# Kernel tuning notes

Measured on AMD Instinct MI355X. Metric: run time of the kernel, lower is better.

Reference implementation:

```python
import jax, jax.numpy as jnp
import numpy as np

N_SRC0, N_DST0 = 500000, 65536
N_DST1 = 8192
E0, E1 = 1048576, 131072
H = 4
SLOPE = 0.2


def gat_conv(h_src, h_dst, src, dst, Ws, Wd, al, ar, b, n_dst, act):
    # h_src: [Ns, Fin], Ws: [Fin, H*D]
    D = Ws.shape[1] // H
    fs = (h_src @ Ws).reshape(-1, H, D)          # [Ns,H,D]
    fd = (h_dst @ Wd).reshape(-1, H, D)          # [Nd,H,D]
    el = jnp.einsum('nhd,hd->nh', fs, al)        # [Ns,H]
    er = jnp.einsum('nhd,hd->nh', fd, ar)        # [Nd,H]
    e = jax.nn.leaky_relu(el[src] + er[dst], SLOPE)   # [E,H]
    m = jax.ops.segment_max(e, dst, num_segments=n_dst, indices_are_sorted=True)
    a = jnp.exp(e - m[dst])                      # [E,H]
    s = jax.ops.segment_sum(a, dst, num_segments=n_dst, indices_are_sorted=True)
    alpha = a / s[dst]                           # [E,H]
    msg = fs[src] * alpha[..., None]             # [E,H,D]
    out = jax.ops.segment_sum(msg, dst, num_segments=n_dst, indices_are_sorted=True) + b
    return act(out)                              # [Nd,H,D]


def setup_inputs() -> dict:
    key = jax.random.key(0)
    ks = jax.random.split(key, 16)
    D0, D1 = 64, 47
    inp = {
        'x': jax.random.normal(ks[0], (N_SRC0, 128), jnp.float32),
        'src0': jax.random.randint(ks[1], (E0,), 0, N_SRC0, jnp.int32),
        'dst0': jnp.sort(jax.random.randint(ks[2], (E0,), 0, N_DST0, jnp.int32)),
        'src1': jax.random.randint(ks[3], (E1,), 0, N_DST0, jnp.int32),
        'dst1': jnp.sort(jax.random.randint(ks[4], (E1,), 0, N_DST1, jnp.int32)),
        'Ws0': jax.random.normal(ks[5], (128, H * D0), jnp.float32) * 0.05,
        'Wd0': jax.random.normal(ks[6], (128, H * D0), jnp.float32) * 0.05,
        'al0': jax.random.normal(ks[7], (H, D0), jnp.float32) * 0.05,
        'ar0': jax.random.normal(ks[8], (H, D0), jnp.float32) * 0.05,
        'b0': jax.random.normal(ks[9], (H, D0), jnp.float32) * 0.05,
        'Ws1': jax.random.normal(ks[10], (H * D0, H * D1), jnp.float32) * 0.05,
        'Wd1': jax.random.normal(ks[11], (H * D0, H * D1), jnp.float32) * 0.05,
        'al1': jax.random.normal(ks[12], (H, D1), jnp.float32) * 0.05,
        'ar1': jax.random.normal(ks[13], (H, D1), jnp.float32) * 0.05,
        'b1': jax.random.normal(ks[14], (H, D1), jnp.float32) * 0.05,
    }
    return inp


def reference(x, src0, dst0, src1, dst1, Ws0, Wd0, al0, ar0, b0, Ws1, Wd1, al1, ar1, b1):
    # Layer 0: bipartite GATConv with ReLU, flatten heads
    h_dst = x[:N_DST0]
    h = gat_conv(x, h_dst, src0, dst0, Ws0, Wd0, al0, ar0, b0, N_DST0, jax.nn.relu)
    h = h.reshape(N_DST0, -1)                    # [N_DST0, H*D0]
    # Layer 1: no activation, mean over heads, log_softmax
    h_dst = h[:N_DST1]
    h = gat_conv(h, h_dst, src1, dst1, Ws1, Wd1, al1, ar1, b1, N_DST1, lambda z: z)
    h = h.mean(axis=1)                           # [N_DST1, D1]
    return jax.nn.log_softmax(h, axis=-1)
```

## Files before the change

### kernel.cpp

```cpp
#include <hip/hip_runtime.h>

typedef _Float16 half8  __attribute__((ext_vector_type(8)));
typedef _Float16 half4v __attribute__((ext_vector_type(4)));
typedef float    f32x4  __attribute__((ext_vector_type(4)));

#define GAT_SLOPE 0.2f
#define N_SRC0 500000
#define N_DST0 65536
#define N_DST1 8192
#define E0 1048576
#define E1 131072
#define H 4
#define MAXSEG 80

__device__ __forceinline__ float leaky(float x) { return x >= 0.f ? x : GAT_SLOPE * x; }

__global__ void collapse_kernel(const float* __restrict__ W, const float* __restrict__ a,
                                float* __restrict__ out, int K, int D) {
  int i = blockIdx.x * 256 + threadIdx.x;
  if (i >= K * 4) return;
  int k = i >> 2, h = i & 3;
  int N = 4 * D;
  float s = 0.f;
  for (int d = 0; d < D; ++d) s += W[(size_t)k * N + h * D + d] * a[h * D + d];
  out[i] = s;
}

__global__ void transposeW_kernel(const float* __restrict__ W, _Float16* __restrict__ WT,
                                  int K, int N) {
  int i = blockIdx.x * 256 + threadIdx.x;
  if (i >= N * K) return;
  int nrow = i / K, k = i - nrow * K;
  WT[i] = (_Float16)W[(size_t)k * N + nrow];
}

__global__ void wstack_kernel(const float* __restrict__ W, _Float16* __restrict__ BTs) {
  int i = blockIdx.x * 256 + threadIdx.x;
  int n = i >> 10, kk = i & 1023;
  int h = kk >> 8, k = kk & 255;
  BTs[i] = (n < 47) ? (_Float16)(0.25f * W[(size_t)k * 188 + h * 47 + n]) : (_Float16)0.f;
}

__global__ void wlr_stack_kernel(const float* __restrict__ wl, const float* __restrict__ wr,
                                 _Float16* __restrict__ out, int K) {
  int i = blockIdx.x * 256 + threadIdx.x;
  if (i >= 16 * K) return;
  int n = i / K, k = i - n * K;
  float v = 0.f;
  if (n < 4) v = wl[k * 4 + n];
  else if (n < 8) v = wr[k * 4 + n - 4];
  out[i] = (_Float16)v;
}

__global__ void seg_starts_kernel(const int* __restrict__ dst, int E, int nseg,
                                  int* __restrict__ seg) {
  int i = blockIdx.x * 256 + threadIdx.x;
  if (i > E) return;
  int lo = (i == 0) ? 0 : dst[i - 1] + 1;
  int hi = (i == E) ? nseg : dst[i];
  for (int d = lo; d <= hi; ++d) seg[d] = i;
}

__global__ __launch_bounds__(256) void cvt_elr_mfma_kernel(
    const float* __restrict__ x, const _Float16* __restrict__ WLR,
    _Float16* __restrict__ xh, float* __restrict__ el, float* __restrict__ er,
    int M, int n_dst) {
  __shared__ _Float16 As[128 * 128];
  const int t = threadIdx.x, lane = t & 63, wid = t >> 6;
  const int m0 = blockIdx.x * 128;
  for (int i = 0; i < 8; ++i) {
    int c = t + 256 * i;
    int row = c >> 4, j = c & 15;
    int gr = m0 + row;
    half8 va = {};
    if (gr < M) {
      float4 f0 = *(const float4*)(x + (size_t)gr * 128 + j * 8);
      float4 f1 = *(const float4*)(x + (size_t)gr * 128 + j * 8 + 4);
      va[0] = (_Float16)f0.x; va[1] = (_Float16)f0.y;
      va[2] = (_Float16)f0.z; va[3] = (_Float16)f0.w;
      va[4] = (_Float16)f1.x; va[5] = (_Float16)f1.y;
      va[6] = (_Float16)f1.z; va[7] = (_Float16)f1.w;
      *(half8*)(xh + (size_t)gr * 128 + j * 8) = va;
    }
    *(half8*)(&As[row * 128 + ((j ^ (row & 7)) << 3)]) = va;
  }
  half8 bf[4];
  for (int kc = 0; kc < 4; ++kc)
    bf[kc] = *(const half8*)(WLR + (lane & 15) * 128 + kc * 32 + (lane >> 4) * 8);
  __syncthreads();
  f32x4 acc[2] = {};
  for (int rt = 0; rt < 2; ++rt) {
    int row = (wid * 2 + rt) * 16 + (lane & 15);
    for (int kc = 0; kc < 4; ++kc) {
      int chunk = kc * 4 + (lane >> 4);
      half8 af = *(const half8*)(&As[row * 128 + ((chunk ^ (row & 7)) << 3)]);
      acc[rt] = __builtin_amdgcn_mfma_f32_16x16x32_f16(af, bf[kc], acc[rt], 0, 0, 0);
    }
  }
  int col = lane & 15, quad = lane >> 4;
  for (int rt = 0; rt < 2; ++rt)
    for (int r = 0; r < 4; ++r) {
      int row = m0 + (wid * 2 + rt) * 16 + quad * 4 + r;
      if (row < M) {
        if (col < 4) el[(size_t)row * 4 + col] = acc[rt][r];
        else if (col < 8 && row < n_dst) er[(size_t)row * 4 + col - 4] = acc[rt][r];
      }
    }
}

__global__ __launch_bounds__(128) void agg0x_kernel(
    const int* __restrict__ src, const int* __restrict__ seg,
    const float* __restrict__ el, const float* __restrict__ er,
    const _Float16* __restrict__ xh, _Float16* __restrict__ axh) {
  int n = blockIdx.x;
  int t = threadIdx.x, lane = t & 63, w = t >> 6;
  __shared__ float sc[4][MAXSEG];
  __shared__ int sid[MAXSEG];
  __shared__ float wpart[8];
  __shared__ float part[512];
  int s0 = seg[n], s1 = seg[n + 1], len = s1 - s0;
  float4 erv = *(const float4*)(er + (size_t)n * 4);
  float s4[4] = {};
  for (int idx = t; idx < len; idx += 128) {
    int sidx = src[s0 + idx];
    float4 e4 = *(const float4*)(el + (size_t)sidx * 4);
    float a0 = __expf(leaky(e4.x + erv.x));
    float a1 = __expf(leaky(e4.y + erv.y));
    float a2 = __expf(leaky(e4.z + erv.z));
    float a3 = __expf(leaky(e4.w + erv.w));
    if (idx < MAXSEG) {
      sc[0][idx] = a0; sc[1][idx] = a1; sc[2][idx] = a2; sc[3][idx] = a3;
      sid[idx] = sidx;
    }
    s4[0] += a0; s4[1] += a1; s4[2] += a2; s4[3] += a3;
  }
#pragma unroll
  for (int off = 32; off; off >>= 1)
#pragma unroll
    for (int h = 0; h < 4; ++h) s4[h] += __shfl_xor(s4[h], off);
  if (lane == 0)
#pragma unroll
    for (int h = 0; h < 4; ++h) wpart[w * 4 + h] = s4[h];
  __syncthreads();
  float sinv[4];
#pragma unroll
  for (int h = 0; h < 4; ++h) {
    float sv = wpart[h] + wpart[4 + h];
    sinv[h] = sv > 0.f ? 1.f / sv : 0.f;
  }
  int g = t >> 5, ci = t & 31;
  float A[4][4] = {};
  for (int idx = g; idx < len; idx += 4) {
    float a0, a1, a2, a3;
    int sidx;
    if (idx < MAXSEG) {
      a0 = sc[0][idx]; a1 = sc[1][idx]; a2 = sc[2][idx]; a3 = sc[3][idx];
      sidx = sid[idx];
    } else {
      sidx = src[s0 + idx];
      float4 e4 = *(const float4*)(el + (size_t)sidx * 4);
      a0 = __expf(leaky(e4.x + erv.x));
      a1 = __expf(leaky(e4.y + erv.y));
      a2 = __expf(leaky(e4.z + erv.z));
      a3 = __expf(leaky(e4.w + erv.w));
    }
    half4v xv = *(const half4v*)(xh + (size_t)sidx * 128 + ci * 4);
#pragma unroll
    for (int c = 0; c < 4; ++c) {
      float xc = (float)xv[c];
      A[0][c] += a0 * xc; A[1][c] += a1 * xc; A[2][c] += a2 * xc; A[3][c] += a3 * xc;
    }
  }
#pragma unroll
  for (int h = 0; h < 4; ++h)
#pragma unroll
    for (int c = 0; c < 4; ++c) A[h][c] += __shfl_xor(A[h][c], 32);
  if (w == 1 && lane < 32)
#pragma unroll
    for (int h = 0; h < 4; ++h)
#pragma unroll
      for (int c = 0; c < 4; ++c) part[ci * 16 + h * 4 + c] = A[h][c];
  __syncthreads();
  if (w == 0 && lane < 32) {
#pragma unroll
    for (int h = 0; h < 4; ++h) {
      half4v o;
#pragma unroll
      for (int c = 0; c < 4; ++c)
        o[c] = (_Float16)((A[h][c] + part[ci * 16 + h * 4 + c]) * sinv[h]);
      *(half4v*)(axh + ((size_t)n * 4 + h) * 128 + ci * 4) = o;
    }
  }
}

__global__ __launch_bounds__(128) void agg1x_kernel(
    const int* __restrict__ src, const int* __restrict__ seg,
    const float* __restrict__ el, const float* __restrict__ er,
    const _Float16* __restrict__ h0, _Float16* __restrict__ axh1) {
  int n = blockIdx.x;
  int t = threadIdx.x, lane = t & 63, w = t >> 6;
  __shared__ float sc[4][MAXSEG];
  __shared__ int sid[MAXSEG];
  __shared__ float wpart[8];
  __shared__ float part[1024];
  int s0 = seg[n], s1 = seg[n + 1], len = s1 - s0;
  float4 erv = *(const float4*)(er + (size_t)n * 4);
  float s4[4] = {};
  for (int idx = t; idx < len; idx += 128) {
    int sidx = src[s0 + idx];
    float4 e4 = *(const float4*)(el + (size_t)sidx * 4);
    float a0 = __expf(leaky(e4.x + erv.x));
    float a1 = __expf(leaky(e4.y + erv.y));
    float a2 = __expf(leaky(e4.z + erv.z));
    float a3 = __expf(leaky(e4.w + erv.w));
    if (idx < MAXSEG) {
      sc[0][idx] = a0; sc[1][idx] = a1; sc[2][idx] = a2; sc[3][idx] = a3;
      sid[idx] = sidx;
    }
    s4[0] += a0; s4[1] += a1; s4[2] += a2; s4[3] += a3;
  }
#pragma unroll
  for (int off = 32; off; off >>= 1)
#pragma unroll
    for (int h = 0; h < 4; ++h) s4[h] += __shfl_xor(s4[h], off);
  if (lane == 0)
#pragma unroll
    for (int h = 0; h < 4; ++h) wpart[w * 4 + h] = s4[h];
  __syncthreads();
  float sinv[4];
#pragma unroll
  for (int h = 0; h < 4; ++h) {
    float sv = wpart[h] + wpart[4 + h];
    sinv[h] = sv > 0.f ? 1.f / sv : 0.f;
  }
  int g = t >> 5, ci = t & 31;
  float A[4][8] = {};
  for (int idx = g; idx < len; idx += 4) {
    float a0, a1, a2, a3;
    int sidx;
    if (idx < MAXSEG) {
      a0 = sc[0][idx]; a1 = sc[1][idx]; a2 = sc[2][idx]; a3 = sc[3][idx];
      sidx = sid[idx];
    } else {
      sidx = src[s0 + idx];
      float4 e4 = *(const float4*)(el + (size_t)sidx * 4);
      a0 = __expf(leaky(e4.x + erv.x));
      a1 = __expf(leaky(e4.y + erv.y));
      a2 = __expf(leaky(e4.z + erv.z));
      a3 = __expf(leaky(e4.w + erv.w));
    }
    half8 xv = *(const half8*)(h0 + (size_t)sidx * 256 + ci * 8);
#pragma unroll
    for (int c = 0; c < 8; ++c) {
      float xc = (float)xv[c];
      A[0][c] += a0 * xc; A[1][c] += a1 * xc; A[2][c] += a2 * xc; A[3][c] += a3 * xc;
    }
  }
#pragma unroll
  for (int h = 0; h < 4; ++h)
#pragma unroll
    for (int c = 0; c < 8; ++c) A[h][c] += __shfl_xor(A[h][c], 32);
  if (w == 1 && lane < 32)
#pragma unroll
    for (int h = 0; h < 4; ++h)
#pragma unroll
      for (int c = 0; c < 8; ++c) part[ci * 32 + h * 8 + c] = A[h][c];
  __syncthreads();
  if (w == 0 && lane < 32) {
#pragma unroll
    for (int h = 0; h < 4; ++h) {
      half8 o;
#pragma unroll
      for (int c = 0; c < 8; ++c)
        o[c] = (_Float16)((A[h][c] + part[ci * 32 + h * 8 + c]) * sinv[h]);
      *(half8*)(axh1 + ((size_t)n * 4 + h) * 256 + ci * 8) = o;
    }
  }
}

__global__ __launch_bounds__(256) void gemm_h0_kernel(
    const _Float16* __restrict__ axh, const _Float16* __restrict__ BT,
    const float* __restrict__ b, const float* __restrict__ wl1,
    const float* __restrict__ wr1, _Float16* __restrict__ h0,
    float* __restrict__ el1, float* __restrict__ er1) {
  __shared__ _Float16 As[128 * 128];
  __shared__ _Float16 Bs[64 * 128];
  const int t = threadIdx.x, lane = t & 63, wid = t >> 6;
  const int m0 = blockIdx.x * 128;
  const int cl = lane & 15, quad = lane >> 4;
  const int wm = wid * 32;
  f32x4 el1p[2][4] = {}, er1p[2][4] = {};
  for (int h = 0; h < 4; ++h) {
    for (int i = 0; i < 8; ++i) {
      int c = t + 256 * i, row = c >> 4, j = c & 15;
      int sw = ((j ^ (row & 7)) << 3);
      *(half8*)(&As[row * 128 + sw]) =
          *(const half8*)(axh + ((size_t)(m0 + row) * 4 + h) * 128 + j * 8);
    }
    for (int i = 0; i < 4; ++i) {
      int c = t + 256 * i, row = c >> 4, j = c & 15;
      int sw = ((j ^ (row & 7)) << 3);
      *(half8*)(&Bs[row * 128 + sw]) =
          *(const half8*)(BT + (size_t)(h * 64 + row) * 128 + j * 8);
    }
    __syncthreads();
    f32x4 acc[2][4] = {};
    for (int ks = 0; ks < 4; ++ks) {
      int kc = ks * 4 + quad;
      half8 af[2], bf[4];
      for (int i = 0; i < 2; ++i) {
        int ra = wm + 16 * i + cl;
        af[i] = *(const half8*)(&As[ra * 128 + ((kc ^ (ra & 7)) << 3)]);
      }
      for (int j2 = 0; j2 < 4; ++j2) {
        int rb = 16 * j2 + cl;
        bf[j2] = *(const half8*)(&Bs[rb * 128 + ((kc ^ (rb & 7)) << 3)]);
      }
      for (int i = 0; i < 2; ++i)
        for (int j2 = 0; j2 < 4; ++j2)
          acc[i][j2] = __builtin_amdgcn_mfma_f32_16x16x32_f16(af[i], bf[j2], acc[i][j2], 0, 0, 0);
    }
    __syncthreads();
    for (int j2 = 0; j2 < 4; ++j2) {
      int gcol = h * 64 + 16 * j2 + cl;
      float bias = b[gcol];
      f32x4 wlv = *(const f32x4*)(wl1 + (size_t)gcol * 4);
      f32x4 wrv = *(const f32x4*)(wr1 + (size_t)gcol * 4);
      for (int i = 0; i < 2; ++i) {
        int r0 = m0 + wm + 16 * i + quad * 4;
        for (int r = 0; r < 4; ++r) {
          float v = fmaxf(acc[i][j2][r] + bias, 0.f);
          h0[(size_t)(r0 + r) * 256 + gcol] = (_Float16)v;
          el1p[i][r] += wlv * v;
          er1p[i][r] += wrv * v;
        }
      }
    }
  }
#pragma unroll
  for (int off = 1; off < 16; off <<= 1)
#pragma unroll
    for (int i = 0; i < 2; ++i)
#pragma unroll
      for (int r = 0; r < 4; ++r)
#pragma unroll
        for (int c = 0; c < 4; ++c) {
          el1p[i][r][c] += __shfl_xor(el1p[i][r][c], off);
          er1p[i][r][c] += __shfl_xor(er1p[i][r][c], off);
        }
  if (cl == 0) {
    for (int i = 0; i < 2; ++i)
      for (int r = 0; r < 4; ++r) {
        int row = m0 + wm + 16 * i + quad * 4 + r;
        *(f32x4*)(el1 + (size_t)row * 4) = el1p[i][r];
        if (row < N_DST1) *(f32x4*)(er1 + (size_t)row * 4) = er1p[i][r];
      }
  }
}

__global__ __launch_bounds__(256) void gemm_out_kernel(
    const _Float16* __restrict__ axh1, const _Float16* __restrict__ BTs,
    const float* __restrict__ b1, float* __restrict__ out) {
  __shared__ _Float16 As[64 * 128];
  __shared__ _Float16 Bs[64 * 128];
  const int t = threadIdx.x, lane = t & 63, wid = t >> 6;
  const int m0 = blockIdx.x * 64;
  f32x4 acc[4] = {};
  for (int k0 = 0; k0 < 1024; k0 += 128) {
    for (int i = 0; i < 4; ++i) {
      int c = t + 256 * i, row = c >> 4, j = c & 15;
      int sw = ((j ^ (row & 7)) << 3);
      *(half8*)(&As[row * 128 + sw]) =
          *(const half8*)(axh1 + (size_t)(m0 + row) * 1024 + k0 + j * 8);
      *(half8*)(&Bs[row * 128 + sw]) =
          *(const half8*)(BTs + (size_t)row * 1024 + k0 + j * 8);
    }
    __syncthreads();
    const int wm = wid * 16;
    for (int ks = 0; ks < 4; ++ks) {
      int kc = ks * 4 + (lane >> 4);
      int ra = wm + (lane & 15);
      half8 af = *(const half8*)(&As[ra * 128 + ((kc ^ (ra & 7)) << 3)]);
      for (int j2 = 0; j2 < 4; ++j2) {
        int rb = 16 * j2 + (lane & 15);
        half8 bf = *(const half8*)(&Bs[rb * 128 + ((kc ^ (rb & 7)) << 3)]);
        acc[j2] = __builtin_amdgcn_mfma_f32_16x16x32_f16(af, bf, acc[j2], 0, 0, 0);
      }
    }
    __syncthreads();
  }
  int quad = lane >> 4, cl = lane & 15;
  float bm[3];
  for (int j2 = 0; j2 < 3; ++j2) {
    int col = 16 * j2 + cl;
    bm[j2] = (col < 47) ? 0.25f * (b1[col] + b1[col + 47] + b1[col + 94] + b1[col + 141]) : 0.f;
  }
  for (int r = 0; r < 4; ++r) {
    int row = m0 + wid * 16 + quad * 4 + r;
    float v[3];
    float mx = -1e30f;
    for (int j2 = 0; j2 < 3; ++j2) {
      int col = 16 * j2 + cl;
      v[j2] = acc[j2][r] + bm[j2];
      if (col < 47) mx = fmaxf(mx, v[j2]);
    }
    for (int off = 8; off; off >>= 1) mx = fmaxf(mx, __shfl_xor(mx, off));
    float s = 0.f;
    for (int j2 = 0; j2 < 3; ++j2) {
      int col = 16 * j2 + cl;
      if (col < 47) s += __expf(v[j2] - mx);
    }
    for (int off = 8; off; off >>= 1) s += __shfl_xor(s, off);
    float lse = mx + __logf(s);
    for (int j2 = 0; j2 < 3; ++j2) {
      int col = 16 * j2 + cl;
      if (col < 47) out[(size_t)row * 47 + col] = v[j2] - lse;
    }
  }
}

extern "C" void kernel_launch(void* const* d_in, const int* in_sizes, int n_in,
                              void* d_out, int out_size, void* d_ws, size_t ws_size,
                              hipStream_t stream) {
  const float* x   = (const float*)d_in[0];
  const int* src0  = (const int*)d_in[1];
  const int* dst0  = (const int*)d_in[2];
  const int* src1  = (const int*)d_in[3];
  const int* dst1  = (const int*)d_in[4];
  const float* Ws0 = (const float*)d_in[5];
  const float* Wd0 = (const float*)d_in[6];
  const float* al0 = (const float*)d_in[7];
  const float* ar0 = (const float*)d_in[8];
  const float* b0  = (const float*)d_in[9];
  const float* Ws1 = (const float*)d_in[10];
  const float* Wd1 = (const float*)d_in[11];
  const float* al1 = (const float*)d_in[12];
  const float* ar1 = (const float*)d_in[13];
  const float* b1  = (const float*)d_in[14];

  char* w = (char*)d_ws;
  auto alloc = [&](size_t bytes) {
    char* p = w;
    w += (bytes + 255) & ~(size_t)255;
    return p;
  };
  _Float16* xh   = (_Float16*)alloc((size_t)N_SRC0 * 128 * 2);
  _Float16* axh  = (_Float16*)alloc((size_t)N_DST0 * 512 * 2);
  _Float16* h0   = (_Float16*)alloc((size_t)N_DST0 * 256 * 2);
  _Float16* axh1 = (_Float16*)alloc((size_t)N_DST1 * 1024 * 2);
  float* el0     = (float*)alloc((size_t)N_SRC0 * 4 * 4);
  float* er0     = (float*)alloc((size_t)N_DST0 * 4 * 4);
  float* el1     = (float*)alloc((size_t)N_DST0 * 4 * 4);
  float* er1     = (float*)alloc((size_t)N_DST1 * 4 * 4);
  int* seg0      = (int*)alloc((size_t)(N_DST0 + 1) * 4);
  int* seg1      = (int*)alloc((size_t)(N_DST1 + 1) * 4);
  _Float16* BT0  = (_Float16*)alloc(256 * 128 * 2);
  _Float16* BTs  = (_Float16*)alloc(64 * 1024 * 2);
  _Float16* WLR0 = (_Float16*)alloc(16 * 128 * 2);
  float* wl0     = (float*)alloc(128 * 4 * 4);
  float* wr0     = (float*)alloc(128 * 4 * 4);
  float* wl1     = (float*)alloc(256 * 4 * 4);
  float* wr1     = (float*)alloc(256 * 4 * 4);

  collapse_kernel<<<2, 256, 0, stream>>>(Ws0, al0, wl0, 128, 64);
  collapse_kernel<<<2, 256, 0, stream>>>(Wd0, ar0, wr0, 128, 64);
  collapse_kernel<<<4, 256, 0, stream>>>(Ws1, al1, wl1, 256, 47);
  collapse_kernel<<<4, 256, 0, stream>>>(Wd1, ar1, wr1, 256, 47);
  wlr_stack_kernel<<<8, 256, 0, stream>>>(wl0, wr0, WLR0, 128);
  transposeW_kernel<<<128, 256, 0, stream>>>(Ws0, BT0, 128, 256);
  wstack_kernel<<<256, 256, 0, stream>>>(Ws1, BTs);
  seg_starts_kernel<<<(E0 + 1 + 255) / 256, 256, 0, stream>>>(dst0, E0, N_DST0, seg0);
  seg_starts_kernel<<<(E1 + 1 + 255) / 256, 256, 0, stream>>>(dst1, E1, N_DST1, seg1);
  cvt_elr_mfma_kernel<<<(N_SRC0 + 127) / 128, 256, 0, stream>>>(x, WLR0, xh, el0, er0,
                                                                N_SRC0, N_DST0);
  agg0x_kernel<<<N_DST0, 128, 0, stream>>>(src0, seg0, el0, er0, xh, axh);
  gemm_h0_kernel<<<N_DST0 / 128, 256, 0, stream>>>(axh, BT0, b0, wl1, wr1, h0, el1, er1);
  agg1x_kernel<<<N_DST1, 128, 0, stream>>>(src1, seg1, el1, er1, h0, axh1);
  gemm_out_kernel<<<N_DST1 / 64, 256, 0, stream>>>(axh1, BTs, b1, (float*)d_out);
}
```

Baseline: 616.9 us.

## Precompute edge scores in a separate pass and aggregate one segment per wavefront

Edge attention scores (exp of leaky-relu of el+er) are now computed by a new edge-parallel kernel and stored in an E×4 buffer. The aggregation kernels change from one 128-thread block per destination node, with shared memory and block barriers, to one wavefront per node. The per-edge weights are broadcast with lane shuffles, and the sum reduction stays inside the wave. This removes the LDS staging and __syncthreads and improves scheduling for the short segments, at the cost of an extra kernel launch and a write and re-read of the alpha buffer (about 16 MB for layer 0).

```diff
diff --git a/kernel.cpp b/kernel.cpp
--- a/kernel.cpp
+++ b/kernel.cpp
@@ -11,7 +11,6 @@
 #define E0 1048576
 #define E1 131072
 #define H 4
-#define MAXSEG 80
 
 __device__ __forceinline__ float leaky(float x) { return x >= 0.f ? x : GAT_SLOPE * x; }
 
@@ -59,6 +58,23 @@
   int lo = (i == 0) ? 0 : dst[i - 1] + 1;
   int hi = (i == E) ? nseg : dst[i];
   for (int d = lo; d <= hi; ++d) seg[d] = i;
+}
+
+__global__ __launch_bounds__(256) void score_kernel(
+    const int* __restrict__ src, const int* __restrict__ dst,
+    const float* __restrict__ el, const float* __restrict__ er,
+    float* __restrict__ alpha, int E) {
+  int e = blockIdx.x * 256 + threadIdx.x;
+  if (e >= E) return;
+  int s = src[e], d = dst[e];
+  float4 e4 = *(const float4*)(el + (size_t)s * 4);
+  float4 r4 = *(const float4*)(er + (size_t)d * 4);
+  float4 o;
+  o.x = __expf(leaky(e4.x + r4.x));
+  o.y = __expf(leaky(e4.y + r4.y));
+  o.z = __expf(leaky(e4.z + r4.z));
+  o.w = __expf(leaky(e4.w + r4.w));
+  *(float4*)(alpha + (size_t)e * 4) = o;
 }
 
 __global__ __launch_bounds__(256) void cvt_elr_mfma_kernel(
@@ -108,171 +124,133 @@
     }
 }
 
-__global__ __launch_bounds__(128) void agg0x_kernel(
+__global__ __launch_bounds__(256) void agg0w_kernel(
     const int* __restrict__ src, const int* __restrict__ seg,
-    const float* __restrict__ el, const float* __restrict__ er,
-    const _Float16* __restrict__ xh, _Float16* __restrict__ axh) {
-  int n = blockIdx.x;
-  int t = threadIdx.x, lane = t & 63, w = t >> 6;
-  __shared__ float sc[4][MAXSEG];
-  __shared__ int sid[MAXSEG];
-  __shared__ float wpart[8];
-  __shared__ float part[512];
+    const float* __restrict__ alpha, const _Float16* __restrict__ xh,
+    _Float16* __restrict__ axh) {
+  const int lane = threadIdx.x & 63, w = threadIdx.x >> 6;
+  const int n = blockIdx.x * 4 + w;
   int s0 = seg[n], s1 = seg[n + 1], len = s1 - s0;
-  float4 erv = *(const float4*)(er + (size_t)n * 4);
-  float s4[4] = {};
-  for (int idx = t; idx < len; idx += 128) {
-    int sidx = src[s0 + idx];
-    float4 e4 = *(const float4*)(el + (size_t)sidx * 4);
-    float a0 = __expf(leaky(e4.x + erv.x));
-    float a1 = __expf(leaky(e4.y + erv.y));
-    float a2 = __expf(leaky(e4.z + erv.z));
-    float a3 = __expf(leaky(e4.w + erv.w));
-    if (idx < MAXSEG) {
-      sc[0][idx] = a0; sc[1][idx] = a1; sc[2][idx] = a2; sc[3][idx] = a3;
-      sid[idx] = sidx;
-    }
-    s4[0] += a0; s4[1] += a1; s4[2] += a2; s4[3] += a3;
-  }
-#pragma unroll
-  for (int off = 32; off; off >>= 1)
-#pragma unroll
-    for (int h = 0; h < 4; ++h) s4[h] += __shfl_xor(s4[h], off);
-  if (lane == 0)
-#pragma unroll
-    for (int h = 0; h < 4; ++h) wpart[w * 4 + h] = s4[h];
-  __syncthreads();
+  float a0 = 0.f, a1 = 0.f, a2 = 0.f, a3 = 0.f;
+  float t0 = 0.f, t1 = 0.f, t2 = 0.f, t3 = 0.f;
+  if (lane < len) {
+    float4 v = *(const float4*)(alpha + (size_t)(s0 + lane) * 4);
+    a0 = v.x; a1 = v.y; a2 = v.z; a3 = v.w;
+    t0 = v.x; t1 = v.y; t2 = v.z; t3 = v.w;
+  }
+  for (int idx = 64 + lane; idx < len; idx += 64) {
+    float4 v = *(const float4*)(alpha + (size_t)(s0 + idx) * 4);
+    t0 += v.x; t1 += v.y; t2 += v.z; t3 += v.w;
+  }
+#pragma unroll
+  for (int off = 32; off; off >>= 1) {
+    t0 += __shfl_xor(t0, off); t1 += __shfl_xor(t1, off);
+    t2 += __shfl_xor(t2, off); t3 += __shfl_xor(t3, off);
+  }
   float sinv[4];
-#pragma unroll
-  for (int h = 0; h < 4; ++h) {
-    float sv = wpart[h] + wpart[4 + h];
-    sinv[h] = sv > 0.f ? 1.f / sv : 0.f;
-  }
-  int g = t >> 5, ci = t & 31;
+  sinv[0] = t0 > 0.f ? 1.f / t0 : 0.f;
+  sinv[1] = t1 > 0.f ? 1.f / t1 : 0.f;
+  sinv[2] = t2 > 0.f ? 1.f / t2 : 0.f;
+  sinv[3] = t3 > 0.f ? 1.f / t3 : 0.f;
+  const int g = lane >> 5, ci = lane & 31;
   float A[4][4] = {};
-  for (int idx = g; idx < len; idx += 4) {
-    float a0, a1, a2, a3;
-    int sidx;
-    if (idx < MAXSEG) {
-      a0 = sc[0][idx]; a1 = sc[1][idx]; a2 = sc[2][idx]; a3 = sc[3][idx];
-      sidx = sid[idx];
-    } else {
-      sidx = src[s0 + idx];
-      float4 e4 = *(const float4*)(el + (size_t)sidx * 4);
-      a0 = __expf(leaky(e4.x + erv.x));
-      a1 = __expf(leaky(e4.y + erv.y));
-      a2 = __expf(leaky(e4.z + erv.z));
-      a3 = __expf(leaky(e4.w + erv.w));
-    }
-    half4v xv = *(const half4v*)(xh + (size_t)sidx * 128 + ci * 4);
-#pragma unroll
-    for (int c = 0; c < 4; ++c) {
-      float xc = (float)xv[c];
-      A[0][c] += a0 * xc; A[1][c] += a1 * xc; A[2][c] += a2 * xc; A[3][c] += a3 * xc;
+  int iters = (len + 1) >> 1;
+  for (int k = 0; k < iters; ++k) {
+    int idx = g + 2 * k;
+    int sl = idx < 64 ? idx : 0;
+    float ah0 = __shfl(a0, sl), ah1 = __shfl(a1, sl);
+    float ah2 = __shfl(a2, sl), ah3 = __shfl(a3, sl);
+    if (idx >= 64 && idx < len) {
+      float4 v = *(const float4*)(alpha + (size_t)(s0 + idx) * 4);
+      ah0 = v.x; ah1 = v.y; ah2 = v.z; ah3 = v.w;
+    }
+    if (idx < len) {
+      int sidx = src[s0 + idx];
+      half4v xv = *(const half4v*)(xh + (size_t)sidx * 128 + ci * 4);
+#pragma unroll
+      for (int c = 0; c < 4; ++c) {
+        float xc = (float)xv[c];
+        A[0][c] += ah0 * xc; A[1][c] += ah1 * xc;
+        A[2][c] += ah2 * xc; A[3][c] += ah3 * xc;
+      }
     }
   }
 #pragma unroll
   for (int h = 0; h < 4; ++h)
 #pragma unroll
     for (int c = 0; c < 4; ++c) A[h][c] += __shfl_xor(A[h][c], 32);
-  if (w == 1 && lane < 32)
-#pragma unroll
-    for (int h = 0; h < 4; ++h)
-#pragma unroll
-      for (int c = 0; c < 4; ++c) part[ci * 16 + h * 4 + c] = A[h][c];
-  __syncthreads();
-  if (w == 0 && lane < 32) {
+  if (g == 0) {
 #pragma unroll
     for (int h = 0; h < 4; ++h) {
       half4v o;
 #pragma unroll
-      for (int c = 0; c < 4; ++c)
-        o[c] = (_Float16)((A[h][c] + part[ci * 16 + h * 4 + c]) * sinv[h]);
+      for (int c = 0; c < 4; ++c) o[c] = (_Float16)(A[h][c] * sinv[h]);
       *(half4v*)(axh + ((size_t)n * 4 + h) * 128 + ci * 4) = o;
     }
   }
 }
 
-__global__ __launch_bounds__(128) void agg1x_kernel(
+__global__ __launch_bounds__(256) void agg1w_kernel(
     const int* __restrict__ src, const int* __restrict__ seg,
-    const float* __restrict__ el, const float* __restrict__ er,
-    const _Float16* __restrict__ h0, _Float16* __restrict__ axh1) {
-  int n = blockIdx.x;
-  int t = threadIdx.x, lane = t & 63, w = t >> 6;
-  __shared__ float sc[4][MAXSEG];
-  __shared__ int sid[MAXSEG];
-  __shared__ float wpart[8];
-  __shared__ float part[1024];
+    const float* __restrict__ alpha, const _Float16* __restrict__ h0,
+    _Float16* __restrict__ axh1) {
+  const int lane = threadIdx.x & 63, w = threadIdx.x >> 6;
+  const int n = blockIdx.x * 4 + w;
   int s0 = seg[n], s1 = seg[n + 1], len = s1 - s0;
-  float4 erv = *(const float4*)(er + (size_t)n * 4);
-  float s4[4] = {};
-  for (int idx = t; idx < len; idx += 128) {
-    int sidx = src[s0 + idx];
-    float4 e4 = *(const float4*)(el + (size_t)sidx * 4);
-    float a0 = __expf(leaky(e4.x + erv.x));
-    float a1 = __expf(leaky(e4.y + erv.y));
-    float a2 = __expf(leaky(e4.z + erv.z));
-    float a3 = __expf(leaky(e4.w + erv.w));
-    if (idx < MAXSEG) {
-      sc[0][idx] = a0; sc[1][idx] = a1; sc[2][idx] = a2; sc[3][idx] = a3;
-      sid[idx] = sidx;
-    }
-    s4[0] += a0; s4[1] += a1; s4[2] += a2; s4[3] += a3;
-  }
-#pragma unroll
-  for (int off = 32; off; off >>= 1)
-#pragma unroll
-    for (int h = 0; h < 4; ++h) s4[h] += __shfl_xor(s4[h], off);
-  if (lane == 0)
-#pragma unroll
-    for (int h = 0; h < 4; ++h) wpart[w * 4 + h] = s4[h];
-  __syncthreads();
+  float a0 = 0.f, a1 = 0.f, a2 = 0.f, a3 = 0.f;
+  float t0 = 0.f, t1 = 0.f, t2 = 0.f, t3 = 0.f;
+  if (lane < len) {
+    float4 v = *(const float4*)(alpha + (size_t)(s0 + lane) * 4);
+    a0 = v.x; a1 = v.y; a2 = v.z; a3 = v.w;
+    t0 = v.x; t1 = v.y; t2 = v.z; t3 = v.w;
+  }
+  for (int idx = 64 + lane; idx < len; idx += 64) {
+    float4 v = *(const float4*)(alpha + (size_t)(s0 + idx) * 4);
+    t0 += v.x; t1 += v.y; t2 += v.z; t3 += v.w;
+  }
+#pragma unroll
+  for (int off = 32; off; off >>= 1) {
+    t0 += __shfl_xor(t0, off); t1 += __shfl_xor(t1, off);
+    t2 += __shfl_xor(t2, off); t3 += __shfl_xor(t3, off);
+  }
   float sinv[4];
-#pragma unroll
-  for (int h = 0; h < 4; ++h) {
-    float sv = wpart[h] + wpart[4 + h];
-    sinv[h] = sv > 0.f ? 1.f / sv : 0.f;
-  }
-  int g = t >> 5, ci = t & 31;
+  sinv[0] = t0 > 0.f ? 1.f / t0 : 0.f;
+  sinv[1] = t1 > 0.f ? 1.f / t1 : 0.f;
+  sinv[2] = t2 > 0.f ? 1.f / t2 : 0.f;
+  sinv[3] = t3 > 0.f ? 1.f / t3 : 0.f;
+  const int g = lane >> 5, ci = lane & 31;
   float A[4][8] = {};
-  for (int idx = g; idx < len; idx += 4) {
-    float a0, a1, a2, a3;
-    int sidx;
-    if (idx < MAXSEG) {
-      a0 = sc[0][idx]; a1 = sc[1][idx]; a2 = sc[2][idx]; a3 = sc[3][idx];
-      sidx = sid[idx];
-    } else {
-      sidx = src[s0 + idx];
-      float4 e4 = *(const float4*)(el + (size_t)sidx * 4);
-      a0 = __expf(leaky(e4.x + erv.x));
-      a1 = __expf(leaky(e4.y + erv.y));
-      a2 = __expf(leaky(e4.z + erv.z));
-      a3 = __expf(leaky(e4.w + erv.w));
-    }
-    half8 xv = *(const half8*)(h0 + (size_t)sidx * 256 + ci * 8);
-#pragma unroll
-    for (int c = 0; c < 8; ++c) {
-      float xc = (float)xv[c];
-      A[0][c] += a0 * xc; A[1][c] += a1 * xc; A[2][c] += a2 * xc; A[3][c] += a3 * xc;
+  int iters = (len + 1) >> 1;
+  for (int k = 0; k < iters; ++k) {
+    int idx = g + 2 * k;
+    int sl = idx < 64 ? idx : 0;
+    float ah0 = __shfl(a0, sl), ah1 = __shfl(a1, sl);
+    float ah2 = __shfl(a2, sl), ah3 = __shfl(a3, sl);
+    if (idx >= 64 && idx < len) {
+      float4 v = *(const float4*)(alpha + (size_t)(s0 + idx) * 4);
+      ah0 = v.x; ah1 = v.y; ah2 = v.z; ah3 = v.w;
+    }
+    if (idx < len) {
+      int sidx = src[s0 + idx];
+      half8 xv = *(const half8*)(h0 + (size_t)sidx * 256 + ci * 8);
+#pragma unroll
+      for (int c = 0; c < 8; ++c) {
+        float xc = (float)xv[c];
+        A[0][c] += ah0 * xc; A[1][c] += ah1 * xc;
+        A[2][c] += ah2 * xc; A[3][c] += ah3 * xc;
+      }
     }
   }
 #pragma unroll
   for (int h = 0; h < 4; ++h)
 #pragma unroll
     for (int c = 0; c < 8; ++c) A[h][c] += __shfl_xor(A[h][c], 32);
-  if (w == 1 && lane < 32)
-#pragma unroll
-    for (int h = 0; h < 4; ++h)
-#pragma unroll
-      for (int c = 0; c < 8; ++c) part[ci * 32 + h * 8 + c] = A[h][c];
-  __syncthreads();
-  if (w == 0 && lane < 32) {
+  if (g == 0) {
 #pragma unroll
     for (int h = 0; h < 4; ++h) {
       half8 o;
 #pragma unroll
-      for (int c = 0; c < 8; ++c)
-        o[c] = (_Float16)((A[h][c] + part[ci * 32 + h * 8 + c]) * sinv[h]);
+      for (int c = 0; c < 8; ++c) o[c] = (_Float16)(A[h][c] * sinv[h]);
       *(half8*)(axh1 + ((size_t)n * 4 + h) * 256 + ci * 8) = o;
     }
   }
@@ -452,6 +430,8 @@
   float* er0     = (float*)alloc((size_t)N_DST0 * 4 * 4);
   float* el1     = (float*)alloc((size_t)N_DST0 * 4 * 4);
   float* er1     = (float*)alloc((size_t)N_DST1 * 4 * 4);
+  float* alpha0  = (float*)alloc((size_t)E0 * 4 * 4);
+  float* alpha1  = (float*)alloc((size_t)E1 * 4 * 4);
   int* seg0      = (int*)alloc((size_t)(N_DST0 + 1) * 4);
   int* seg1      = (int*)alloc((size_t)(N_DST1 + 1) * 4);
   _Float16* BT0  = (_Float16*)alloc(256 * 128 * 2);
@@ -473,8 +453,10 @@
   seg_starts_kernel<<<(E1 + 1 + 255) / 256, 256, 0, stream>>>(dst1, E1, N_DST1, seg1);
   cvt_elr_mfma_kernel<<<(N_SRC0 + 127) / 128, 256, 0, stream>>>(x, WLR0, xh, el0, er0,
                                                                 N_SRC0, N_DST0);
-  agg0x_kernel<<<N_DST0, 128, 0, stream>>>(src0, seg0, el0, er0, xh, axh);
+  score_kernel<<<E0 / 256, 256, 0, stream>>>(src0, dst0, el0, er0, alpha0, E0);
+  agg0w_kernel<<<N_DST0 / 4, 256, 0, stream>>>(src0, seg0, alpha0, xh, axh);
   gemm_h0_kernel<<<N_DST0 / 128, 256, 0, stream>>>(axh, BT0, b0, wl1, wr1, h0, el1, er1);
-  agg1x_kernel<<<N_DST1, 128, 0, stream>>>(src1, seg1, el1, er1, h0, axh1);
+  score_kernel<<<E1 / 256, 256, 0, stream>>>(src1, dst1, el1, er1, alpha1, E1);
+  agg1w_kernel<<<N_DST1 / 4, 256, 0, stream>>>(src1, seg1, alpha1, h0, axh1);
   gemm_out_kernel<<<N_DST1 / 64, 256, 0, stream>>>(axh1, BTs, b1, (float*)d_out);
 }
```

New measurement: 641.7 us. +4.0%, slower.
